# Optimization experiments

Hardware: AMD Instinct MI355X
Metric: run time of the kernel (lower is better)

Reference implementation:

```python
import jax, jax.numpy as jnp
import numpy as np

DIM = 1024
HEADS = 16
SCALE = DIM ** -0.5  # NOTE: original scales by full dim, not head dim


def setup_inputs() -> dict:
    key = jax.random.key(0)
    ks = jax.random.split(key, 6)
    B, S, D = 2, 2048, DIM
    x = jax.random.normal(ks[0], (B, S, D), dtype=jnp.float32)
    Wq = jax.random.normal(ks[1], (D, D), dtype=jnp.float32) * 0.02
    Wk = jax.random.normal(ks[2], (D, D), dtype=jnp.float32) * 0.02
    Wv = jax.random.normal(ks[3], (D, D), dtype=jnp.float32) * 0.02
    Wo = jax.random.normal(ks[4], (D, D), dtype=jnp.float32) * 0.02
    z = jnp.zeros((D,), dtype=jnp.float32)
    return {"x": x, "Wq": Wq, "bq": z, "Wk": Wk, "bk": z, "Wv": Wv, "bv": z, "Wo": Wo, "bo": z}


def reference(x, Wq, bq, Wk, bk, Wv, bv, Wo, bo):
    B, S, D = x.shape
    H = HEADS
    d = D // H
    # projections (Linear: x @ W + b)
    q = (x @ Wq + bq).reshape(B, S, H, d).transpose(0, 2, 1, 3)  # b h i d
    k = (x @ Wk + bk).reshape(B, S, H, d).transpose(0, 2, 1, 3)  # b h j d
    v = (x @ Wv + bv).reshape(B, S, H, d).transpose(0, 2, 1, 3)  # b h j d
    dots = jnp.einsum("bhid,bhjd->bhij", q, k) * SCALE
    # causal mask: strict upper triangle -> -inf
    mask = jnp.triu(jnp.ones((S, S), dtype=bool), k=1)
    dots = jnp.where(mask, -jnp.inf, dots)
    attn = jax.nn.softmax(dots, axis=-1)
    out = jnp.einsum("bhij,bhjd->bhid", attn, v)
    out = out.transpose(0, 2, 1, 3).reshape(B, S, D)  # b i (h d)
    return out @ Wo + bo
```

## Files before the change

### kernel.cpp

```cpp
#include <hip/hip_runtime.h>
#include <hip/hip_bf16.h>

typedef __bf16 bf16;
typedef __bf16 bf16x4 __attribute__((ext_vector_type(4)));
typedef __bf16 bf16x8 __attribute__((ext_vector_type(8)));
typedef float floatx4 __attribute__((ext_vector_type(4)));

#define MFMA_16x16x32(a, b, c) __builtin_amdgcn_mfma_f32_16x16x32_bf16((a), (b), (c), 0, 0, 0)
#define NEG_INF (-__builtin_inff())

#define CB 2
#define CS 2048
#define CD 1024
#define CH 16
#define CM (CB * CS)
#define QSC (0.03125f * 1.44269504088896340736f)

__device__ __forceinline__ void async16(const bf16* g, bf16* l) {
    __builtin_amdgcn_global_load_lds(
        (const __attribute__((address_space(1))) void*)g,
        (__attribute__((address_space(3))) void*)l, 16, 0, 0);
}

__global__ __launch_bounds__(256) void conv_x(const float* __restrict__ x,
                                              bf16* __restrict__ xb) {
    size_t i = ((size_t)blockIdx.x * 256 + threadIdx.x) * 8;
    float4 a = *(const float4*)(x + i);
    float4 b = *(const float4*)(x + i + 4);
    bf16x8 v;
    v[0] = (bf16)a.x; v[1] = (bf16)a.y; v[2] = (bf16)a.z; v[3] = (bf16)a.w;
    v[4] = (bf16)b.x; v[5] = (bf16)b.y; v[6] = (bf16)b.z; v[7] = (bf16)b.w;
    *(bf16x8*)(xb + i) = v;
}

__global__ __launch_bounds__(256) void conv_wt(
    const float* __restrict__ W0, const float* __restrict__ W1,
    const float* __restrict__ W2, const float* __restrict__ W3,
    bf16* __restrict__ Wt) {
    __shared__ bf16 Ws[64 * 68];
    const float* W = blockIdx.z == 0 ? W0 : blockIdx.z == 1 ? W1
                   : blockIdx.z == 2 ? W2 : W3;
    bf16* out = Wt + (size_t)blockIdx.z * CD * CD;
    const int t = threadIdx.x;
    const int n0 = blockIdx.x * 64, k0 = blockIdx.y * 64;
    const int rr = t >> 4, c4 = (t & 15) * 4;
#pragma unroll
    for (int i = 0; i < 4; i++) {
        int r = rr + i * 16;
        float4 f = *(const float4*)(W + (size_t)(k0 + r) * CD + n0 + c4);
        bf16x4 v;
        v[0] = (bf16)f.x; v[1] = (bf16)f.y; v[2] = (bf16)f.z; v[3] = (bf16)f.w;
        *(bf16x4*)&Ws[r * 68 + c4] = v;
    }
    __syncthreads();
#pragma unroll
    for (int i = 0; i < 4; i++) {
        int n = rr + i * 16;
        bf16x4 v;
#pragma unroll
        for (int j = 0; j < 4; j++) v[j] = Ws[(c4 + j) * 68 + n];
        *(bf16x4*)(out + (size_t)(n0 + n) * CD + k0 + c4) = v;
    }
}

__global__ __launch_bounds__(256) void gemm_qkv(
    const bf16* __restrict__ A, const bf16* __restrict__ Bt,
    const float* __restrict__ bq, const float* __restrict__ bk,
    const float* __restrict__ bv,
    bf16* __restrict__ Qb, bf16* __restrict__ Kb, bf16* __restrict__ Vb) {
    __shared__ bf16 As[128 * 32];
    __shared__ bf16 Bs[128 * 32];
    const int t = threadIdx.x, w = t >> 6, lane = t & 63;
    const int quad = lane >> 4, l15 = lane & 15;
    const int which = blockIdx.x >> 3;
    const int bn = (blockIdx.x & 7) * 128, bm = blockIdx.y * 128;
    const bf16* Bw = Bt + (size_t)which * CD * CD;

    const bf16* ag = A + (size_t)(bm + w * 16 + (lane >> 2)) * CD + (lane & 3) * 8;
    const bf16* bg = Bw + (size_t)(bn + w * 16 + (lane >> 2)) * CD + (lane & 3) * 8;
    const int lo = w * 16 * 32;

    const int wm = (w >> 1) * 64, wn = (w & 1) * 64;
    floatx4 acc[4][4] = {};

    for (int k0 = 0; k0 < CD; k0 += 32) {
        async16(ag + k0, &As[lo]);
        async16(ag + (size_t)64 * CD + k0, &As[lo + 64 * 32]);
        async16(bg + k0, &Bs[lo]);
        async16(bg + (size_t)64 * CD + k0, &Bs[lo + 64 * 32]);
        __syncthreads();
        bf16x8 af[4], bfr[4];
#pragma unroll
        for (int mt = 0; mt < 4; mt++)
            af[mt] = *(const bf16x8*)&As[(wm + mt * 16 + l15) * 32 + quad * 8];
#pragma unroll
        for (int nt = 0; nt < 4; nt++)
            bfr[nt] = *(const bf16x8*)&Bs[(wn + nt * 16 + l15) * 32 + quad * 8];
#pragma unroll
        for (int mt = 0; mt < 4; mt++)
#pragma unroll
            for (int nt = 0; nt < 4; nt++)
                acc[mt][nt] = MFMA_16x16x32(af[mt], bfr[nt], acc[mt][nt]);
        __syncthreads();
    }

    const float* bias = which == 0 ? bq : which == 1 ? bk : bv;
    bf16* out = which == 0 ? Qb : Kb;
#pragma unroll
    for (int mt = 0; mt < 4; mt++) {
#pragma unroll
        for (int nt = 0; nt < 4; nt++) {
            int token = bm + wm + mt * 16 + quad * 4;
            int col = bn + wn + nt * 16 + l15;
            int b = token >> 11, s = token & (CS - 1);
            int h = col >> 6, dd = col & 63;
            if (which == 2) {
                bf16x4 pv;
#pragma unroll
                for (int r = 0; r < 4; r++) pv[r] = (bf16)(acc[mt][nt][r] + bias[col]);
                *(bf16x4*)&Vb[(((size_t)(b * CH + h)) * 64 + dd) * CS + s] = pv;
            } else {
#pragma unroll
                for (int r = 0; r < 4; r++) {
                    float v = acc[mt][nt][r] + bias[col];
                    if (which == 0) v *= QSC;
                    out[(((size_t)(b * CH + h)) * CS + s + r) * 64 + dd] = (bf16)v;
                }
            }
        }
    }
}

__global__ __launch_bounds__(256) void gemm_o(
    const bf16* __restrict__ A, const bf16* __restrict__ Bt,
    const float* __restrict__ bias, float* __restrict__ out) {
    __shared__ bf16 As[64 * 32];
    __shared__ bf16 Bs[128 * 32];
    const int t = threadIdx.x, w = t >> 6, lane = t & 63;
    const int quad = lane >> 4, l15 = lane & 15;
    const int bn = blockIdx.x * 128, bm = blockIdx.y * 64;

    const bf16* ag = A + (size_t)(bm + w * 16 + (lane >> 2)) * CD + (lane & 3) * 8;
    const bf16* bg = Bt + (size_t)(bn + w * 16 + (lane >> 2)) * CD + (lane & 3) * 8;
    const int lo = w * 16 * 32;

    const int wm = (w >> 1) * 32, wn = (w & 1) * 64;
    floatx4 acc[2][4] = {};

    for (int k0 = 0; k0 < CD; k0 += 32) {
        async16(ag + k0, &As[lo]);
        async16(bg + k0, &Bs[lo]);
        async16(bg + (size_t)64 * CD + k0, &Bs[lo + 64 * 32]);
        __syncthreads();
        bf16x8 af[2], bfr[4];
#pragma unroll
        for (int mt = 0; mt < 2; mt++)
            af[mt] = *(const bf16x8*)&As[(wm + mt * 16 + l15) * 32 + quad * 8];
#pragma unroll
        for (int nt = 0; nt < 4; nt++)
            bfr[nt] = *(const bf16x8*)&Bs[(wn + nt * 16 + l15) * 32 + quad * 8];
#pragma unroll
        for (int mt = 0; mt < 2; mt++)
#pragma unroll
            for (int nt = 0; nt < 4; nt++)
                acc[mt][nt] = MFMA_16x16x32(af[mt], bfr[nt], acc[mt][nt]);
        __syncthreads();
    }

#pragma unroll
    for (int mt = 0; mt < 2; mt++)
#pragma unroll
        for (int nt = 0; nt < 4; nt++)
#pragma unroll
            for (int r = 0; r < 4; r++) {
                int row = bm + wm + mt * 16 + quad * 4 + r;
                int col = bn + wn + nt * 16 + l15;
                out[(size_t)row * CD + col] = acc[mt][nt][r] + bias[col];
            }
}

__global__ __launch_bounds__(256) void attn_kernel(
    const bf16* __restrict__ Q, const bf16* __restrict__ Kg,
    const bf16* __restrict__ Vg, bf16* __restrict__ Ob) {
    __shared__ bf16 Ks[2][64 * 72];
    __shared__ bf16 Vt[2][64 * 72];
    __shared__ bf16 Pt[4][32 * 72];

    const int t = threadIdx.x;
    const int w = t >> 6, lane = t & 63;
    const int quad = lane >> 4, l15 = lane & 15;

    const int half = blockIdx.x >> 8;
    const int slot = blockIdx.x & 255;
    const int bh   = slot & 31;
    const int qq   = slot >> 5;
    const int qb   = half ? qq : (15 - qq);
    const int q0   = qb * 128;
    const int wrow0 = q0 + w * 32;
    const int nT = 2 * qb + 2;

    const bf16* Qh = Q + (size_t)bh * CS * 64;
    const bf16* Kh = Kg + (size_t)bh * CS * 64;
    const bf16* Vh = Vg + (size_t)bh * 64 * CS;

    const int strow = t >> 2, soff = (t & 3) * 16;
    const bf16* ksrc = Kh + (size_t)strow * 64 + soff;
    const bf16* vsrc = Vh + (size_t)strow * CS + soff;
    const int sbase = strow * 72 + soff;

    bf16x8 kr0 = *(const bf16x8*)ksrc;
    bf16x8 kr1 = *(const bf16x8*)(ksrc + 8);
    bf16x8 vr0 = *(const bf16x8*)vsrc;
    bf16x8 vr1 = *(const bf16x8*)(vsrc + 8);
    *(bf16x8*)&Ks[0][sbase]     = kr0;
    *(bf16x8*)&Ks[0][sbase + 8] = kr1;
    *(bf16x8*)&Vt[0][sbase]     = vr0;
    *(bf16x8*)&Vt[0][sbase + 8] = vr1;
    kr0 = *(const bf16x8*)(ksrc + 64 * 64);
    kr1 = *(const bf16x8*)(ksrc + 64 * 64 + 8);
    vr0 = *(const bf16x8*)(vsrc + 64);
    vr1 = *(const bf16x8*)(vsrc + 64 + 8);

    bf16x8 qf[2][2];
#pragma unroll
    for (int g = 0; g < 2; g++) {
        const bf16* qsrc = Qh + (size_t)(wrow0 + g * 16 + l15) * 64 + quad * 8;
        qf[g][0] = *(const bf16x8*)qsrc;
        qf[g][1] = *(const bf16x8*)(qsrc + 32);
    }

    floatx4 o[4][2] = {};
    float m_r[2] = {NEG_INF, NEG_INF};
    float l_r[2] = {0.f, 0.f};

    bf16* pw = Pt[w];

    for (int kt = 0; kt < nT; kt++) {
        const int cur = kt & 1;
        const int ks0 = kt * 64;
        __syncthreads();

        *(bf16x8*)&Ks[cur ^ 1][sbase]     = kr0;
        *(bf16x8*)&Ks[cur ^ 1][sbase + 8] = kr1;
        *(bf16x8*)&Vt[cur ^ 1][sbase]     = vr0;
        *(bf16x8*)&Vt[cur ^ 1][sbase + 8] = vr1;
        {
            int nk = (kt + 2 < nT) ? kt + 2 : 0;
            const bf16* kn = ksrc + (size_t)nk * 64 * 64;
            const bf16* vn = vsrc + nk * 64;
            kr0 = *(const bf16x8*)kn;
            kr1 = *(const bf16x8*)(kn + 8);
            vr0 = *(const bf16x8*)vn;
            vr1 = *(const bf16x8*)(vn + 8);
        }
        if (ks0 > wrow0 + 31) continue;

        const bf16* ksb = Ks[cur];
        const bf16* vtb = Vt[cur];

        floatx4 sc[2][4] = {};
        __builtin_amdgcn_s_setprio(1);
#pragma unroll
        for (int nt = 0; nt < 4; nt++) {
            bf16x8 af0 = *(const bf16x8*)&ksb[(nt * 16 + l15) * 72 + quad * 8];
            bf16x8 af1 = *(const bf16x8*)&ksb[(nt * 16 + l15) * 72 + 32 + quad * 8];
#pragma unroll
            for (int g = 0; g < 2; g++) {
                sc[g][nt] = MFMA_16x16x32(af0, qf[g][0], sc[g][nt]);
                sc[g][nt] = MFMA_16x16x32(af1, qf[g][1], sc[g][nt]);
            }
        }
        __builtin_amdgcn_s_setprio(0);
        if (ks0 + 63 > wrow0) {
#pragma unroll
            for (int g = 0; g < 2; g++) {
                int qrow = wrow0 + g * 16 + l15;
#pragma unroll
                for (int nt = 0; nt < 4; nt++)
#pragma unroll
                    for (int r = 0; r < 4; r++)
                        if (ks0 + nt * 16 + quad * 4 + r > qrow)
                            sc[g][nt][r] = NEG_INF;
            }
        }
        float mx[2];
#pragma unroll
        for (int g = 0; g < 2; g++) {
            float m = NEG_INF;
#pragma unroll
            for (int nt = 0; nt < 4; nt++)
#pragma unroll
                for (int r = 0; r < 4; r++) m = fmaxf(m, sc[g][nt][r]);
            m = fmaxf(m, __shfl_xor(m, 16));
            m = fmaxf(m, __shfl_xor(m, 32));
            mx[g] = m;
        }
        int need = (mx[0] > m_r[0] + 8.f) || (mx[1] > m_r[1] + 8.f);
        if (__any(need)) {
#pragma unroll
            for (int g = 0; g < 2; g++) {
                float mn = fmaxf(m_r[g], mx[g]);
                float a = __builtin_amdgcn_exp2f(m_r[g] - mn);
                m_r[g] = mn;
                l_r[g] *= a;
#pragma unroll
                for (int dt = 0; dt < 4; dt++)
#pragma unroll
                    for (int r = 0; r < 4; r++) o[dt][g][r] *= a;
            }
        }
#pragma unroll
        for (int g = 0; g < 2; g++) {
            float s = 0.f;
#pragma unroll
            for (int nt = 0; nt < 4; nt++)
#pragma unroll
                for (int r = 0; r < 4; r++) {
                    sc[g][nt][r] = __builtin_amdgcn_exp2f(sc[g][nt][r] - m_r[g]);
                    s += sc[g][nt][r];
                }
            l_r[g] += s;
        }
#pragma unroll
        for (int g = 0; g < 2; g++)
#pragma unroll
            for (int nt = 0; nt < 4; nt++) {
                bf16x4 pk;
#pragma unroll
                for (int r = 0; r < 4; r++) pk[r] = (bf16)sc[g][nt][r];
                *(bf16x4*)&pw[(g * 16 + l15) * 72 + nt * 16 + quad * 4] = pk;
            }
        bf16x8 bp[2][2];
#pragma unroll
        for (int g = 0; g < 2; g++) {
            bp[g][0] = *(const bf16x8*)&pw[(g * 16 + l15) * 72 + quad * 8];
            bp[g][1] = *(const bf16x8*)&pw[(g * 16 + l15) * 72 + 32 + quad * 8];
        }
        __builtin_amdgcn_s_setprio(1);
#pragma unroll
        for (int dt = 0; dt < 4; dt++) {
            bf16x8 av0 = *(const bf16x8*)&vtb[(dt * 16 + l15) * 72 + quad * 8];
            bf16x8 av1 = *(const bf16x8*)&vtb[(dt * 16 + l15) * 72 + 32 + quad * 8];
#pragma unroll
            for (int g = 0; g < 2; g++) {
                o[dt][g] = MFMA_16x16x32(av0, bp[g][0], o[dt][g]);
                o[dt][g] = MFMA_16x16x32(av1, bp[g][1], o[dt][g]);
            }
        }
        __builtin_amdgcn_s_setprio(0);
    }

    const int b = bh >> 4, h = bh & 15;
#pragma unroll
    for (int g = 0; g < 2; g++) {
        float l = l_r[g];
        l += __shfl_xor(l, 16);
        l += __shfl_xor(l, 32);
        float rl = 1.f / l;
        int row = wrow0 + g * 16 + l15;
#pragma unroll
        for (int dt = 0; dt < 4; dt++) {
            bf16x4 ov;
#pragma unroll
            for (int r = 0; r < 4; r++) ov[r] = (bf16)(o[dt][g][r] * rl);
            *(bf16x4*)&Ob[((size_t)b * CS + row) * CD + h * 64 + dt * 16 + quad * 4] = ov;
        }
    }
}

extern "C" void kernel_launch(void* const* d_in, const int* in_sizes, int n_in,
                              void* d_out, int out_size, void* d_ws, size_t ws_size,
                              hipStream_t stream) {
    const float* x  = (const float*)d_in[0];
    const float* Wq = (const float*)d_in[1];
    const float* bq = (const float*)d_in[2];
    const float* Wk = (const float*)d_in[3];
    const float* bk = (const float*)d_in[4];
    const float* Wv = (const float*)d_in[5];
    const float* bv = (const float*)d_in[6];
    const float* Wo = (const float*)d_in[7];
    const float* bo = (const float*)d_in[8];
    float* out = (float*)d_out;

    bf16* xb = (bf16*)d_ws;
    bf16* Wt = xb + (size_t)CM * CD;
    bf16* Qb = Wt + (size_t)4 * CD * CD;
    bf16* Kb = Qb + (size_t)CB * CH * CS * 64;
    bf16* Vb = Kb + (size_t)CB * CH * CS * 64;
    bf16* Ob = Vb + (size_t)CB * CH * CS * 64;

    conv_x<<<(CM * CD) / (256 * 8), 256, 0, stream>>>(x, xb);
    conv_wt<<<dim3(CD / 64, CD / 64, 4), 256, 0, stream>>>(Wq, Wk, Wv, Wo, Wt);

    gemm_qkv<<<dim3(24, CM / 128), 256, 0, stream>>>(
        xb, Wt, bq, bk, bv, Qb, Kb, Vb);

    attn_kernel<<<512, 256, 0, stream>>>(Qb, Kb, Vb, Ob);

    gemm_o<<<dim3(8, CM / 64), 256, 0, stream>>>(
        Ob, Wt + (size_t)3 * CD * CD, bo, out);
}
```

Before: 191.7 us.

## Split KV tiles across two wave groups per attention block and merge

The attention kernel now launches 512 threads per block, with two groups of four waves. Each group takes alternating 64-wide KV tiles for the same 128 query rows, using its own double-buffered K/V shared memory. At the end the partial softmax state (m, l, O) is merged through shared memory reused from the K buffers. This halves the serial KV loop length per block to shorten the critical path of the causal-imbalanced blocks. The cost is higher LDS use per block, which may reduce concurrent blocks, plus an extra merge step; max and sum reductions are also rewritten as trees.

```diff
diff --git a/kernel.cpp b/kernel.cpp
--- a/kernel.cpp
+++ b/kernel.cpp
@@ -179,47 +179,53 @@
             }
 }
 
-__global__ __launch_bounds__(256) void attn_kernel(
+__global__ __launch_bounds__(512) void attn_kernel(
     const bf16* __restrict__ Q, const bf16* __restrict__ Kg,
     const bf16* __restrict__ Vg, bf16* __restrict__ Ob) {
-    __shared__ bf16 Ks[2][64 * 72];
-    __shared__ bf16 Vt[2][64 * 72];
-    __shared__ bf16 Pt[4][32 * 72];
+    __shared__ bf16 Ks[2][2][64 * 72];
+    __shared__ bf16 Vt[2][2][64 * 72];
+    __shared__ bf16 Pt[8][32 * 72];
 
     const int t = threadIdx.x;
     const int w = t >> 6, lane = t & 63;
+    const int grp = w >> 2, wg = w & 3;
     const int quad = lane >> 4, l15 = lane & 15;
 
-    const int half = blockIdx.x >> 8;
-    const int slot = blockIdx.x & 255;
-    const int bh   = slot & 31;
-    const int qq   = slot >> 5;
-    const int qb   = half ? qq : (15 - qq);
-    const int q0   = qb * 128;
-    const int wrow0 = q0 + w * 32;
+    const int qb = 15 - (blockIdx.x >> 5);
+    const int bh = blockIdx.x & 31;
+    const int q0 = qb * 128;
+    const int wrow0 = q0 + wg * 32;
     const int nT = 2 * qb + 2;
+    const int nS = nT >> 1;
 
     const bf16* Qh = Q + (size_t)bh * CS * 64;
     const bf16* Kh = Kg + (size_t)bh * CS * 64;
     const bf16* Vh = Vg + (size_t)bh * 64 * CS;
 
-    const int strow = t >> 2, soff = (t & 3) * 16;
+    const int tl = t & 255;
+    const int strow = tl >> 2, soff = (tl & 3) * 16;
     const bf16* ksrc = Kh + (size_t)strow * 64 + soff;
     const bf16* vsrc = Vh + (size_t)strow * CS + soff;
     const int sbase = strow * 72 + soff;
 
-    bf16x8 kr0 = *(const bf16x8*)ksrc;
-    bf16x8 kr1 = *(const bf16x8*)(ksrc + 8);
-    bf16x8 vr0 = *(const bf16x8*)vsrc;
-    bf16x8 vr1 = *(const bf16x8*)(vsrc + 8);
-    *(bf16x8*)&Ks[0][sbase]     = kr0;
-    *(bf16x8*)&Ks[0][sbase + 8] = kr1;
-    *(bf16x8*)&Vt[0][sbase]     = vr0;
-    *(bf16x8*)&Vt[0][sbase + 8] = vr1;
-    kr0 = *(const bf16x8*)(ksrc + 64 * 64);
-    kr1 = *(const bf16x8*)(ksrc + 64 * 64 + 8);
-    vr0 = *(const bf16x8*)(vsrc + 64);
-    vr1 = *(const bf16x8*)(vsrc + 64 + 8);
+    {
+        const bf16* k0p = ksrc + (size_t)grp * 64 * 64;
+        const bf16* v0p = vsrc + grp * 64;
+        bf16x8 a = *(const bf16x8*)k0p, b = *(const bf16x8*)(k0p + 8);
+        bf16x8 c = *(const bf16x8*)v0p, d = *(const bf16x8*)(v0p + 8);
+        *(bf16x8*)&Ks[grp][0][sbase]     = a;
+        *(bf16x8*)&Ks[grp][0][sbase + 8] = b;
+        *(bf16x8*)&Vt[grp][0][sbase]     = c;
+        *(bf16x8*)&Vt[grp][0][sbase + 8] = d;
+    }
+    bf16x8 kr0, kr1, vr0, vr1;
+    {
+        int t1 = (grp + 2 < nT) ? grp + 2 : 0;
+        const bf16* kn = ksrc + (size_t)t1 * 64 * 64;
+        const bf16* vn = vsrc + t1 * 64;
+        kr0 = *(const bf16x8*)kn;  kr1 = *(const bf16x8*)(kn + 8);
+        vr0 = *(const bf16x8*)vn;  vr1 = *(const bf16x8*)(vn + 8);
+    }
 
     bf16x8 qf[2][2];
 #pragma unroll
@@ -235,28 +241,27 @@
 
     bf16* pw = Pt[w];
 
-    for (int kt = 0; kt < nT; kt++) {
-        const int cur = kt & 1;
-        const int ks0 = kt * 64;
+    for (int s = 0; s < nS; s++) {
+        const int tile = 2 * s + grp;
+        const int cur = s & 1;
+        const int ks0 = tile * 64;
         __syncthreads();
 
-        *(bf16x8*)&Ks[cur ^ 1][sbase]     = kr0;
-        *(bf16x8*)&Ks[cur ^ 1][sbase + 8] = kr1;
-        *(bf16x8*)&Vt[cur ^ 1][sbase]     = vr0;
-        *(bf16x8*)&Vt[cur ^ 1][sbase + 8] = vr1;
+        *(bf16x8*)&Ks[grp][cur ^ 1][sbase]     = kr0;
+        *(bf16x8*)&Ks[grp][cur ^ 1][sbase + 8] = kr1;
+        *(bf16x8*)&Vt[grp][cur ^ 1][sbase]     = vr0;
+        *(bf16x8*)&Vt[grp][cur ^ 1][sbase + 8] = vr1;
         {
-            int nk = (kt + 2 < nT) ? kt + 2 : 0;
+            int nk = (tile + 4 < nT) ? tile + 4 : 0;
             const bf16* kn = ksrc + (size_t)nk * 64 * 64;
             const bf16* vn = vsrc + nk * 64;
-            kr0 = *(const bf16x8*)kn;
-            kr1 = *(const bf16x8*)(kn + 8);
-            vr0 = *(const bf16x8*)vn;
-            vr1 = *(const bf16x8*)(vn + 8);
+            kr0 = *(const bf16x8*)kn;  kr1 = *(const bf16x8*)(kn + 8);
+            vr0 = *(const bf16x8*)vn;  vr1 = *(const bf16x8*)(vn + 8);
         }
         if (ks0 > wrow0 + 31) continue;
 
-        const bf16* ksb = Ks[cur];
-        const bf16* vtb = Vt[cur];
+        const bf16* ksb = Ks[grp][cur];
+        const bf16* vtb = Vt[grp][cur];
 
         floatx4 sc[2][4] = {};
         __builtin_amdgcn_s_setprio(1);
@@ -286,11 +291,14 @@
         float mx[2];
 #pragma unroll
         for (int g = 0; g < 2; g++) {
-            float m = NEG_INF;
-#pragma unroll
-            for (int nt = 0; nt < 4; nt++)
-#pragma unroll
-                for (int r = 0; r < 4; r++) m = fmaxf(m, sc[g][nt][r]);
+            floatx4 v01, v23, vm;
+#pragma unroll
+            for (int c = 0; c < 4; c++) {
+                v01[c] = fmaxf(sc[g][0][c], sc[g][1][c]);
+                v23[c] = fmaxf(sc[g][2][c], sc[g][3][c]);
+                vm[c] = fmaxf(v01[c], v23[c]);
+            }
+            float m = fmaxf(fmaxf(vm[0], vm[1]), fmaxf(vm[2], vm[3]));
             m = fmaxf(m, __shfl_xor(m, 16));
             m = fmaxf(m, __shfl_xor(m, 32));
             mx[g] = m;
@@ -311,15 +319,13 @@
         }
 #pragma unroll
         for (int g = 0; g < 2; g++) {
-            float s = 0.f;
 #pragma unroll
             for (int nt = 0; nt < 4; nt++)
 #pragma unroll
-                for (int r = 0; r < 4; r++) {
+                for (int r = 0; r < 4; r++)
                     sc[g][nt][r] = __builtin_amdgcn_exp2f(sc[g][nt][r] - m_r[g]);
-                    s += sc[g][nt][r];
-                }
-            l_r[g] += s;
+            floatx4 st = (sc[g][0] + sc[g][1]) + (sc[g][2] + sc[g][3]);
+            l_r[g] += (st[0] + st[1]) + (st[2] + st[3]);
         }
 #pragma unroll
         for (int g = 0; g < 2; g++)
@@ -350,20 +356,53 @@
         __builtin_amdgcn_s_setprio(0);
     }
 
-    const int b = bh >> 4, h = bh & 15;
-#pragma unroll
-    for (int g = 0; g < 2; g++) {
-        float l = l_r[g];
-        l += __shfl_xor(l, 16);
-        l += __shfl_xor(l, 32);
-        float rl = 1.f / l;
-        int row = wrow0 + g * 16 + l15;
-#pragma unroll
-        for (int dt = 0; dt < 4; dt++) {
-            bf16x4 ov;
-#pragma unroll
-            for (int r = 0; r < 4; r++) ov[r] = (bf16)(o[dt][g][r] * rl);
-            *(bf16x4*)&Ob[((size_t)b * CS + row) * CD + h * 64 + dt * 16 + quad * 4] = ov;
+    __syncthreads();
+    float* mg = (float*)&Ks[0][0][0];
+    float* base = mg + (size_t)(wg * 64 + lane) * 36;
+    if (grp == 1) {
+#pragma unroll
+        for (int dt = 0; dt < 4; dt++)
+#pragma unroll
+            for (int g = 0; g < 2; g++)
+                *(floatx4*)(base + (dt * 2 + g) * 4) = o[dt][g];
+        base[32] = m_r[0]; base[33] = m_r[1];
+        base[34] = l_r[0]; base[35] = l_r[1];
+    }
+    __syncthreads();
+    if (grp == 0) {
+        float a0[2], a1[2];
+#pragma unroll
+        for (int g = 0; g < 2; g++) {
+            float m1 = base[32 + g], l1 = base[34 + g];
+            float mm = fmaxf(m_r[g], m1);
+            a0[g] = __builtin_amdgcn_exp2f(m_r[g] - mm);
+            a1[g] = __builtin_amdgcn_exp2f(m1 - mm);
+            l_r[g] = l_r[g] * a0[g] + l1 * a1[g];
+        }
+#pragma unroll
+        for (int dt = 0; dt < 4; dt++)
+#pragma unroll
+            for (int g = 0; g < 2; g++) {
+                floatx4 o1 = *(const floatx4*)(base + (dt * 2 + g) * 4);
+#pragma unroll
+                for (int r = 0; r < 4; r++)
+                    o[dt][g][r] = o[dt][g][r] * a0[g] + o1[r] * a1[g];
+            }
+        const int b = bh >> 4, h = bh & 15;
+#pragma unroll
+        for (int g = 0; g < 2; g++) {
+            float l = l_r[g];
+            l += __shfl_xor(l, 16);
+            l += __shfl_xor(l, 32);
+            float rl = 1.f / l;
+            int row = wrow0 + g * 16 + l15;
+#pragma unroll
+            for (int dt = 0; dt < 4; dt++) {
+                bf16x4 ov;
+#pragma unroll
+                for (int r = 0; r < 4; r++) ov[r] = (bf16)(o[dt][g][r] * rl);
+                *(bf16x4*)&Ob[((size_t)b * CS + row) * CD + h * 64 + dt * 16 + quad * 4] = ov;
+            }
         }
     }
 }
@@ -395,7 +434,7 @@
     gemm_qkv<<<dim3(24, CM / 128), 256, 0, stream>>>(
         xb, Wt, bq, bk, bv, Qb, Kb, Vb);
 
-    attn_kernel<<<512, 256, 0, stream>>>(Qb, Kb, Vb, Ob);
+    attn_kernel<<<512, 512, 0, stream>>>(Qb, Kb, Vb, Ob);
 
     gemm_o<<<dim3(8, CM / 64), 256, 0, stream>>>(
         Ob, Wt + (size_t)3 * CD * CD, bo, out);
```

Result: faster. 181.8 us, median of 2 (-5.1%).
